# Optimization experiments

Hardware: AMD Instinct MI355X
Metric: run time of the kernel (lower is better)

The kernel has to match this reference:

```python
import jax, jax.numpy as jnp
import numpy as np

N_GENE, N_DIS = 100_000, 50_000   # node counts per node type
D = 128                            # hidden_channels (= input dim, required by skipsum)
E = 800_000                        # edges per edge type
L = 2                              # num_layers
EPS = 1e-12                        # torch F.normalize eps


def setup_inputs() -> dict:
    key = jax.random.key(0)
    ks = jax.random.split(key, 9)
    s = 1.0 / np.sqrt(D)
    return {
        "x_gene": jax.random.normal(ks[0], (N_GENE, D), jnp.float32),
        "x_disease": jax.random.normal(ks[1], (N_DIS, D), jnp.float32),
        # per (layer, edge_type) SAGEConv weights: lin_l (neighbors), lin_r (root), bias
        # edge_type 0: gene->disease, edge_type 1: disease->gene
        "Wl": jax.random.normal(ks[2], (L, 2, D, D), jnp.float32) * s,
        "Wr": jax.random.normal(ks[3], (L, 2, D, D), jnp.float32) * s,
        "b": jax.random.normal(ks[4], (L, 2, D), jnp.float32) * 0.01,
        "src_g2d": jax.random.randint(ks[5], (E,), 0, N_GENE, dtype=jnp.int32),
        "dst_g2d": jax.random.randint(ks[6], (E,), 0, N_DIS, dtype=jnp.int32),
        "src_d2g": jax.random.randint(ks[7], (E,), 0, N_DIS, dtype=jnp.int32),
        "dst_d2g": jax.random.randint(ks[8], (E,), 0, N_GENE, dtype=jnp.int32),
    }


def _sage(x_src, x_dst, src, dst, Wl, Wr, b, n_dst):
    # SAGEConv with aggr='mean': lin_l(mean_{j in N(i)} x_j) + lin_r(x_i) + bias
    msg = jnp.take(x_src, src, axis=0)                                   # [E, D] gather
    summed = jax.ops.segment_sum(msg, dst, num_segments=n_dst)           # [n_dst, D]
    cnt = jax.ops.segment_sum(jnp.ones_like(src, dtype=x_src.dtype), dst,
                              num_segments=n_dst)                        # [n_dst]
    mean = summed / jnp.maximum(cnt, 1.0)[:, None]                       # isolated nodes -> 0
    return mean @ Wl.T + x_dst @ Wr.T + b


def _l2norm(x):
    n = jnp.linalg.norm(x, axis=-1, keepdims=True)
    return x / jnp.maximum(n, EPS)


def reference(x_gene, x_disease, Wl, Wr, b, src_g2d, dst_g2d, src_d2g, dst_d2g):
    xg, xd = x_gene, x_disease
    for i in range(L):
        # to_hetero: one conv per edge type; macro_aggregation='sum' across edge types
        # (each dst type here receives exactly one edge type)
        hd = _sage(xg, xd, src_g2d, dst_g2d, Wl[i, 0], Wr[i, 0], b[i, 0], N_DIS)
        hg = _sage(xd, xg, src_d2g, dst_d2g, Wl[i, 1], Wr[i, 1], b[i, 1], N_GENE)
        if i < L - 1:  # hidden layers get the activation
            hg, hd = jax.nn.relu(hg), jax.nn.relu(hd)
        # L2_norm=True -> normalize every layer
        hg, hd = _l2norm(hg), _l2norm(hd)
        # skipsum
        xg, xd = hg + xg, hd + xd
    return xg, xd
```

## Files before the change

kernel.cpp:

```cpp
#include <hip/hip_runtime.h>
#include <math.h>

#define NG 100000
#define ND 50000
#define NTOT 150000
#define DIM 128
#define NE 800000
#define EPSN 1e-12f

#define RPB 256
#define NBT_D2 196
#define NBT_G2 391

#define NBK 586
#define SCB 128
#define EPB 12500

typedef __bf16 bf16x8 __attribute__((ext_vector_type(8)));
typedef float f32x4 __attribute__((ext_vector_type(4)));
typedef unsigned int uint32;

__device__ __forceinline__ ushort rne_bf16(float f) {
  uint32 u = __builtin_bit_cast(uint32, f);
  u += 0x7fffu + ((u >> 16) & 1u);
  return (ushort)(u >> 16);
}


__global__ void zero_ints(int* __restrict__ p, int n) {
  int i = blockIdx.x * 256 + threadIdx.x;
  if (i < n) p[i] = 0;
}

__global__ void bucket_count(const int* __restrict__ dst_g2d, const int* __restrict__ dst_d2g,
                             int* __restrict__ bcnt) {
  __shared__ int h[NBK];
  for (int j = threadIdx.x; j < NBK; j += 256) h[j] = 0;
  __syncthreads();
  int stride = gridDim.x * 256;
  for (int i = blockIdx.x * 256 + threadIdx.x; i < 2 * NE; i += stride) {
    int d = (i < NE) ? dst_g2d[i] : ND + dst_d2g[i - NE];
    atomicAdd(&h[d >> 8], 1);
  }
  __syncthreads();
  for (int j = threadIdx.x; j < NBK; j += 256)
    if (h[j]) atomicAdd(&bcnt[j], h[j]);
}

__global__ void bucket_scan(const int* __restrict__ bcnt, int* __restrict__ bbase,
                            int* __restrict__ bcur) {
  __shared__ int s[1024];
  int t = threadIdx.x;
  s[t] = (t < NBK) ? bcnt[t] : 0;
  __syncthreads();
  for (int off = 1; off < 1024; off <<= 1) {
    int v = (t >= off) ? s[t - off] : 0;
    __syncthreads();
    s[t] += v;
    __syncthreads();
  }
  if (t < NBK) {
    int e = (t > 0) ? s[t - 1] : 0;
    bbase[t] = e;
    bcur[t] = e;
  }
  if (t == 0) bbase[NBK] = 2 * NE;
}

__global__ void bucket_scatter(const int* __restrict__ src_g2d, const int* __restrict__ dst_g2d,
                               const int* __restrict__ src_d2g, const int* __restrict__ dst_d2g,
                               int* __restrict__ bcur, int2* __restrict__ pairs) {
  __shared__ int h[NBK];
  __shared__ int base[NBK];
  int e0 = blockIdx.x * EPB;
  int e1 = e0 + EPB;
  if (e1 > 2 * NE) e1 = 2 * NE;
  for (int j = threadIdx.x; j < NBK; j += 256) h[j] = 0;
  __syncthreads();
  for (int i = e0 + threadIdx.x; i < e1; i += 256) {
    int d = (i < NE) ? dst_g2d[i] : ND + dst_d2g[i - NE];
    atomicAdd(&h[d >> 8], 1);
  }
  __syncthreads();
  for (int j = threadIdx.x; j < NBK; j += 256) {
    int c = h[j];
    base[j] = c ? atomicAdd(&bcur[j], c) : 0;
    h[j] = 0;
  }
  __syncthreads();
  for (int i = e0 + threadIdx.x; i < e1; i += 256) {
    int d, s;
    if (i < NE) {
      d = dst_g2d[i];
      s = src_g2d[i];
    } else {
      d = ND + dst_d2g[i - NE];
      s = src_d2g[i - NE];
    }
    int bkt = d >> 8;
    int p = base[bkt] + atomicAdd(&h[bkt], 1);
    pairs[p] = make_int2(d, s);
  }
}

__global__ void bucket_to_csr(const int* __restrict__ bbase, const int2* __restrict__ pairs,
                              int* __restrict__ off, int* __restrict__ csr) {
  __shared__ int cnt[256];
  __shared__ int ss[256];
  int b = blockIdx.x, t = threadIdx.x;
  int n0 = b << 8;
  int s0 = bbase[b], s1 = bbase[b + 1];
  cnt[t] = 0;
  __syncthreads();
  for (int i = s0 + t; i < s1; i += 256) atomicAdd(&cnt[pairs[i].x - n0], 1);
  __syncthreads();
  int x = cnt[t];
  ss[t] = x;
  __syncthreads();
  for (int o = 1; o < 256; o <<= 1) {
    int y = (t >= o) ? ss[t - o] : 0;
    __syncthreads();
    ss[t] += y;
    __syncthreads();
  }
  int abs0 = s0 + ss[t] - x;
  int node = n0 + t;
  if (node < NTOT) off[node] = abs0;
  if (node == NTOT - 1) off[NTOT] = 2 * NE;
  __syncthreads();
  cnt[t] = abs0;
  __syncthreads();
  for (int i = s0 + t; i < s1; i += 256) {
    int2 e = pairs[i];
    int p = atomicAdd(&cnt[e.x - n0], 1);
    csr[p] = e.y;
  }
}


__global__ void to_bf16_all(const float* __restrict__ xg, const float* __restrict__ xd,
                            ushort* __restrict__ yg, ushort* __restrict__ yd) {
  int i = blockIdx.x * 256 + threadIdx.x;
  if (i >= NTOT * 16) return;
  const float* x;
  ushort* y;
  int j;
  if (i < NG * 16) {
    x = xg; y = yg; j = i;
  } else {
    x = xd; y = yd; j = i - NG * 16;
  }
  const float4* px = (const float4*)x;
  float4 a = px[2 * j], b = px[2 * j + 1];
  float v[8] = {a.x, a.y, a.z, a.w, b.x, b.y, b.z, b.w};
  uint32 u[4];
#pragma unroll
  for (int k = 0; k < 4; k++)
    u[k] = (uint32)rne_bf16(v[2 * k]) | ((uint32)rne_bf16(v[2 * k + 1]) << 16);
  ((int4*)y)[j] = make_int4((int)u[0], (int)u[1], (int)u[2], (int)u[3]);
}


__global__ void split_w(const float* __restrict__ Wl, const float* __restrict__ Wr,
                        ushort* __restrict__ WlH, ushort* __restrict__ WlL,
                        ushort* __restrict__ WrH, ushort* __restrict__ WrL) {
  int i = blockIdx.x * 256 + threadIdx.x;
  if (i >= 4 * 128 * 128) return;
  {
    float a = Wl[i];
    uint32 u = __builtin_bit_cast(uint32, a);
    float hf = __builtin_bit_cast(float, u & 0xffff0000u);
    WlH[i] = (ushort)(u >> 16);
    WlL[i] = (ushort)(__builtin_bit_cast(uint32, a - hf) >> 16);
  }
  {
    float a = Wr[i];
    uint32 u = __builtin_bit_cast(uint32, a);
    float hf = __builtin_bit_cast(float, u & 0xffff0000u);
    WrH[i] = (ushort)(u >> 16);
    WrL[i] = (ushort)(__builtin_bit_cast(uint32, a - hf) >> 16);
  }
}


__device__ __forceinline__ void acc8(float* a, int4 u) {
  uint32 w;
  w = (uint32)u.x;
  a[0] += __builtin_bit_cast(float, w << 16);
  a[1] += __builtin_bit_cast(float, w & 0xffff0000u);
  w = (uint32)u.y;
  a[2] += __builtin_bit_cast(float, w << 16);
  a[3] += __builtin_bit_cast(float, w & 0xffff0000u);
  w = (uint32)u.z;
  a[4] += __builtin_bit_cast(float, w << 16);
  a[5] += __builtin_bit_cast(float, w & 0xffff0000u);
  w = (uint32)u.w;
  a[6] += __builtin_bit_cast(float, w << 16);
  a[7] += __builtin_bit_cast(float, w & 0xffff0000u);
}

__global__ void agg_comb(const ushort* __restrict__ xg_bf, const ushort* __restrict__ xd_bf,
                         const int* __restrict__ off, const int* __restrict__ csr,
                         ushort* __restrict__ agg_bf) {
  int node = (blockIdx.x * 256 + threadIdx.x) >> 6;
  if (node >= NTOT) return;
  int lane = threadIdx.x & 63;
  const ushort* xsrc = (node < ND) ? xg_bf : xd_bf;
  int e0 = off[node], e1 = off[node + 1];
  int q = lane >> 4, l16 = lane & 15;
  const int4* xs = (const int4*)xsrc;
  float a[8] = {0.f, 0.f, 0.f, 0.f, 0.f, 0.f, 0.f, 0.f};
  int e = e0 + q;
  for (; e + 4 < e1; e += 8) {
    int s0 = csr[e], s1 = csr[e + 4];
    int4 u = xs[(size_t)s0 * 16 + l16];
    int4 v = xs[(size_t)s1 * 16 + l16];
    acc8(a, u);
    acc8(a, v);
  }
  if (e < e1) acc8(a, xs[(size_t)csr[e] * 16 + l16]);
#pragma unroll
  for (int j = 0; j < 8; j++) {
    a[j] += __shfl_xor(a[j], 16);
    a[j] += __shfl_xor(a[j], 32);
  }
  if (q == 0) {
    int deg = e1 - e0;
    float inv = (deg > 0) ? 1.f / (float)deg : 0.f;
    uint32 u[4];
#pragma unroll
    for (int j = 0; j < 4; j++)
      u[j] = (uint32)rne_bf16(a[2 * j] * inv) | ((uint32)rne_bf16(a[2 * j + 1] * inv) << 16);
    *(int4*)&agg_bf[(size_t)node * DIM + l16 * 8] =
        make_int4((int)u[0], (int)u[1], (int)u[2], (int)u[3]);
  }
}


__device__ __forceinline__ void split8(const float* xp, bf16x8& hi, bf16x8& lo) {
  float4 f0 = *(const float4*)xp;
  float4 f1 = *(const float4*)(xp + 4);
  float v[8] = {f0.x, f0.y, f0.z, f0.w, f1.x, f1.y, f1.z, f1.w};
  uint32 hw[4], lw[4];
#pragma unroll
  for (int j = 0; j < 4; j++) {
    uint32 u0 = __builtin_bit_cast(uint32, v[2 * j]);
    uint32 u1 = __builtin_bit_cast(uint32, v[2 * j + 1]);
    float hf0 = __builtin_bit_cast(float, u0 & 0xffff0000u);
    float hf1 = __builtin_bit_cast(float, u1 & 0xffff0000u);
    uint32 l0 = __builtin_bit_cast(uint32, v[2 * j] - hf0) >> 16;
    uint32 l1 = __builtin_bit_cast(uint32, v[2 * j + 1] - hf1) >> 16;
    hw[j] = (u0 >> 16) | ((u1 >> 16) << 16);
    lw[j] = l0 | (l1 << 16);
  }
  hi = __builtin_bit_cast(bf16x8, make_int4((int)hw[0], (int)hw[1], (int)hw[2], (int)hw[3]));
  lo = __builtin_bit_cast(bf16x8, make_int4((int)lw[0], (int)lw[1], (int)lw[2], (int)lw[3]));
}

__launch_bounds__(256, 1)
__global__ void sage_dual(const ushort* __restrict__ agg_bf, const float* __restrict__ xd,
                          const float* __restrict__ xg, const ushort* __restrict__ WlH,
                          const ushort* __restrict__ WlL, const ushort* __restrict__ WrH,
                          const ushort* __restrict__ WrL, const float* __restrict__ bias_all,
                          float* __restrict__ outd, float* __restrict__ outg,
                          ushort* __restrict__ xbf_d, ushort* __restrict__ xbf_g, int layer,
                          int relu, int write_bf) {
  __shared__ __align__(16) char smem[131072];

  int b = blockIdx.x;
  const float* X;
  float* O;
  ushort* OBF;
  int n, set, r0g, cbase;
  if (b < NBT_D2) {
    X = xd; O = outd; OBF = xbf_d; n = ND; set = layer * 2; r0g = b * RPB; cbase = 0;
  } else {
    X = xg; O = outg; OBF = xbf_g; n = NG; set = layer * 2 + 1;
    r0g = (b - NBT_D2) * RPB; cbase = ND;
  }
  const ushort* Wplanes[4] = {WlH + set * 16384, WlL + set * 16384, WrH + set * 16384,
                              WrL + set * 16384};
  const float* bias = bias_all + set * 128;

  int tid = threadIdx.x;
  int wave = tid >> 6, lane = tid & 63;
  int m = lane & 15, q = lane >> 4;

#pragma unroll
  for (int i = 0; i < 32; i++) {
    int c = tid + i * 256;
    int p = c >> 11;
    int Bl = (c & 2047) * 16;
    int4 v = *(const int4*)((const char*)Wplanes[p] + Bl);
    int dst = p * 32768 + (Bl ^ (((Bl >> 8) & 7) << 4));
    *(int4*)(smem + dst) = v;
  }
  __syncthreads();

  f32x4 acc[4][8];
#pragma unroll
  for (int mt = 0; mt < 4; mt++)
#pragma unroll
    for (int nt = 0; nt < 8; nt++) acc[mt][nt] = (f32x4)0.f;

  int rb = r0g + wave * 64;

#pragma unroll
  for (int ks = 0; ks < 4; ks++) {
    int kc = ks * 32 + q * 8;
    int kb = ks * 64 + q * 16;
    bf16x8 a[4];
#pragma unroll
    for (int mt = 0; mt < 4; mt++) {
      int r = rb + mt * 16 + m;
      if (r >= n) r = n - 1;
      a[mt] = __builtin_bit_cast(bf16x8, *(const int4*)&agg_bf[(size_t)(cbase + r) * DIM + kc]);
    }
#pragma unroll
    for (int nt = 0; nt < 8; nt++) {
      int nn = nt * 16 + m;
      int wb = (nn * 256 + kb) ^ ((nn & 7) << 4);
      bf16x8 bh = *(const bf16x8*)(smem + wb);
      bf16x8 bl = *(const bf16x8*)(smem + 32768 + wb);
#pragma unroll
      for (int mt = 0; mt < 4; mt++) {
        acc[mt][nt] = __builtin_amdgcn_mfma_f32_16x16x32_bf16(a[mt], bh, acc[mt][nt], 0, 0, 0);
        acc[mt][nt] = __builtin_amdgcn_mfma_f32_16x16x32_bf16(a[mt], bl, acc[mt][nt], 0, 0, 0);
      }
    }
  }

#pragma unroll
  for (int ks = 0; ks < 4; ks++) {
    int kc = ks * 32 + q * 8;
    int kb = ks * 64 + q * 16;
    bf16x8 ah[4], al[4];
#pragma unroll
    for (int mt = 0; mt < 4; mt++) {
      int r = rb + mt * 16 + m;
      if (r >= n) r = n - 1;
      split8(&X[(size_t)r * DIM + kc], ah[mt], al[mt]);
    }
#pragma unroll
    for (int nt = 0; nt < 8; nt++) {
      int nn = nt * 16 + m;
      int wb = (nn * 256 + kb) ^ ((nn & 7) << 4);
      bf16x8 bh = *(const bf16x8*)(smem + 65536 + wb);
      bf16x8 bl = *(const bf16x8*)(smem + 98304 + wb);
#pragma unroll
      for (int mt = 0; mt < 4; mt++) {
        acc[mt][nt] = __builtin_amdgcn_mfma_f32_16x16x32_bf16(ah[mt], bh, acc[mt][nt], 0, 0, 0);
        acc[mt][nt] = __builtin_amdgcn_mfma_f32_16x16x32_bf16(ah[mt], bl, acc[mt][nt], 0, 0, 0);
        acc[mt][nt] = __builtin_amdgcn_mfma_f32_16x16x32_bf16(al[mt], bh, acc[mt][nt], 0, 0, 0);
      }
    }
  }

  __syncthreads();

  float bb[8];
#pragma unroll
  for (int nt = 0; nt < 8; nt++) bb[nt] = bias[nt * 16 + m];

  const int S = 132;
  float* wbuf = (float*)smem + wave * (16 * S);

  int half = lane >> 5;
  int c4 = (lane & 31) * 4;

#pragma unroll
  for (int mt = 0; mt < 4; mt++) {
#pragma unroll
    for (int reg = 0; reg < 4; reg++) {
      float h[8];
      float ss = 0.f;
#pragma unroll
      for (int nt = 0; nt < 8; nt++) {
        float v = acc[mt][nt][reg] + bb[nt];
        if (relu) v = fmaxf(v, 0.f);
        h[nt] = v;
        ss += v * v;
      }
      ss += __shfl_xor(ss, 1);
      ss += __shfl_xor(ss, 2);
      ss += __shfl_xor(ss, 4);
      ss += __shfl_xor(ss, 8);
      float inv = 1.f / fmaxf(sqrtf(ss), EPSN);
      int rrel = q * 4 + reg;
#pragma unroll
      for (int nt = 0; nt < 8; nt++) wbuf[rrel * S + nt * 16 + m] = h[nt] * inv;
    }
#pragma unroll
    for (int i = 0; i < 8; i++) {
      int rrel = i * 2 + half;
      int R = rb + mt * 16 + rrel;
      if (R < n) {
        f32x4 hv = *(const f32x4*)&wbuf[rrel * S + c4];
        float4 xr = *(const float4*)&X[(size_t)R * DIM + c4];
        float4 o;
        o.x = hv[0] + xr.x;
        o.y = hv[1] + xr.y;
        o.z = hv[2] + xr.z;
        o.w = hv[3] + xr.w;
        *(float4*)&O[(size_t)R * DIM + c4] = o;
        if (write_bf) {
          int2 pk = make_int2((int)((uint32)rne_bf16(o.x) | ((uint32)rne_bf16(o.y) << 16)),
                              (int)((uint32)rne_bf16(o.z) | ((uint32)rne_bf16(o.w) << 16)));
          *(int2*)&OBF[(size_t)R * DIM + c4] = pk;
        }
      }
    }
  }
}


extern "C" void kernel_launch(void* const* d_in, const int* in_sizes, int n_in,
                              void* d_out, int out_size, void* d_ws, size_t ws_size,
                              hipStream_t stream) {
  const float* xg0 = (const float*)d_in[0];
  const float* xd0 = (const float*)d_in[1];
  const float* Wl = (const float*)d_in[2];
  const float* Wr = (const float*)d_in[3];
  const float* bs = (const float*)d_in[4];
  const int* src_g2d = (const int*)d_in[5];
  const int* dst_g2d = (const int*)d_in[6];
  const int* src_d2g = (const int*)d_in[7];
  const int* dst_d2g = (const int*)d_in[8];

  float* out_xg = (float*)d_out;
  float* out_xd = (float*)d_out + (size_t)NG * DIM;

  char* p = (char*)d_ws;
  auto alloc = [&](size_t bytes) -> char* {
    char* q = p;
    p += (bytes + 255) & ~(size_t)255;
    return q;
  };
  int* off = (int*)alloc((NTOT + 1) * 4);
  int* csr = (int*)alloc((size_t)2 * NE * 4);
  int* bcnt = (int*)alloc(NBK * 4);
  int* bbase = (int*)alloc((NBK + 1) * 4);
  int* bcur = (int*)alloc(NBK * 4);
  char* big = alloc((size_t)NTOT * DIM * 2);
  int2* pairs = (int2*)big;
  ushort* agg_bf = (ushort*)big;
  ushort* xg_bf = (ushort*)alloc((size_t)NG * DIM * 2);
  ushort* xd_bf = (ushort*)alloc((size_t)ND * DIM * 2);
  ushort* WlH = (ushort*)alloc((size_t)4 * 128 * 128 * 2);
  ushort* WlL = (ushort*)alloc((size_t)4 * 128 * 128 * 2);
  ushort* WrH = (ushort*)alloc((size_t)4 * 128 * 128 * 2);
  ushort* WrL = (ushort*)alloc((size_t)4 * 128 * 128 * 2);

  const int TB = 256;

  split_w<<<256, TB, 0, stream>>>(Wl, Wr, WlH, WlL, WrH, WrL);
  to_bf16_all<<<(NTOT * 16 + TB - 1) / TB, TB, 0, stream>>>(xg0, xd0, xg_bf, xd_bf);

  zero_ints<<<(NBK + TB - 1) / TB, TB, 0, stream>>>(bcnt, NBK);
  bucket_count<<<256, TB, 0, stream>>>(dst_g2d, dst_d2g, bcnt);
  bucket_scan<<<1, 1024, 0, stream>>>(bcnt, bbase, bcur);
  bucket_scatter<<<SCB, TB, 0, stream>>>(src_g2d, dst_g2d, src_d2g, dst_d2g, bcur, pairs);
  bucket_to_csr<<<NBK, TB, 0, stream>>>(bbase, pairs, off, csr);

  int aggBlocks = NTOT / 4;
  int sageBlocks = NBT_D2 + NBT_G2;

  agg_comb<<<aggBlocks, TB, 0, stream>>>(xg_bf, xd_bf, off, csr, agg_bf);
  sage_dual<<<sageBlocks, TB, 0, stream>>>(agg_bf, xd0, xg0, WlH, WlL, WrH, WrL, bs, out_xd,
                                           out_xg, xd_bf, xg_bf, 0, 1, 1);

  agg_comb<<<aggBlocks, TB, 0, stream>>>(xg_bf, xd_bf, off, csr, agg_bf);
  sage_dual<<<sageBlocks, TB, 0, stream>>>(agg_bf, out_xd, out_xg, WlH, WlL, WrH, WrL, bs,
                                           out_xd, out_xg, xd_bf, xg_bf, 1, 0, 0);
}
```

Before: 539.3 us.

## Use 16 lanes per node in aggregation and halve sage LDS for two blocks/CU

The aggregation kernel now assigns one 16-lane group per destination node instead of a full 64-lane wave, walking edges sequentially with 4-way unrolled gathers and no cross-lane shuffle reduction. The sage_dual kernel stages only the Wl planes into shared memory first, then restages the Wr planes into the same 64 KB buffer, with extra barriers in between. Halving the LDS footprint and raising launch_bounds to 2 blocks per CU is meant to improve occupancy and latency hiding. The cost is an extra weight reload and more barriers per block, plus tighter register limits that could cause spills.

Measured after the change: 483.6 us. 1.12x faster.

```diff
diff --git a/kernel.cpp b/kernel.cpp
--- a/kernel.cpp
+++ b/kernel.cpp
@@ -202,38 +202,40 @@
 __global__ void agg_comb(const ushort* __restrict__ xg_bf, const ushort* __restrict__ xd_bf,
                          const int* __restrict__ off, const int* __restrict__ csr,
                          ushort* __restrict__ agg_bf) {
-  int node = (blockIdx.x * 256 + threadIdx.x) >> 6;
+  int node = (blockIdx.x * 256 + threadIdx.x) >> 4;
   if (node >= NTOT) return;
-  int lane = threadIdx.x & 63;
-  const ushort* xsrc = (node < ND) ? xg_bf : xd_bf;
+  int l16 = threadIdx.x & 15;
+  const int4* xs = (const int4*)((node < ND) ? xg_bf : xd_bf);
   int e0 = off[node], e1 = off[node + 1];
-  int q = lane >> 4, l16 = lane & 15;
-  const int4* xs = (const int4*)xsrc;
   float a[8] = {0.f, 0.f, 0.f, 0.f, 0.f, 0.f, 0.f, 0.f};
-  int e = e0 + q;
-  for (; e + 4 < e1; e += 8) {
-    int s0 = csr[e], s1 = csr[e + 4];
-    int4 u = xs[(size_t)s0 * 16 + l16];
-    int4 v = xs[(size_t)s1 * 16 + l16];
-    acc8(a, u);
-    acc8(a, v);
+  int e = e0;
+  for (; e + 3 < e1; e += 4) {
+    int s0 = csr[e], s1 = csr[e + 1], s2 = csr[e + 2], s3 = csr[e + 3];
+    int4 v0 = xs[(size_t)s0 * 16 + l16];
+    int4 v1 = xs[(size_t)s1 * 16 + l16];
+    int4 v2 = xs[(size_t)s2 * 16 + l16];
+    int4 v3 = xs[(size_t)s3 * 16 + l16];
+    acc8(a, v0);
+    acc8(a, v1);
+    acc8(a, v2);
+    acc8(a, v3);
+  }
+  for (; e + 1 < e1; e += 2) {
+    int s0 = csr[e], s1 = csr[e + 1];
+    int4 v0 = xs[(size_t)s0 * 16 + l16];
+    int4 v1 = xs[(size_t)s1 * 16 + l16];
+    acc8(a, v0);
+    acc8(a, v1);
   }
   if (e < e1) acc8(a, xs[(size_t)csr[e] * 16 + l16]);
-#pragma unroll
-  for (int j = 0; j < 8; j++) {
-    a[j] += __shfl_xor(a[j], 16);
-    a[j] += __shfl_xor(a[j], 32);
-  }
-  if (q == 0) {
-    int deg = e1 - e0;
-    float inv = (deg > 0) ? 1.f / (float)deg : 0.f;
-    uint32 u[4];
-#pragma unroll
-    for (int j = 0; j < 4; j++)
-      u[j] = (uint32)rne_bf16(a[2 * j] * inv) | ((uint32)rne_bf16(a[2 * j + 1] * inv) << 16);
-    *(int4*)&agg_bf[(size_t)node * DIM + l16 * 8] =
-        make_int4((int)u[0], (int)u[1], (int)u[2], (int)u[3]);
-  }
+  int deg = e1 - e0;
+  float inv = (deg > 0) ? 1.f / (float)deg : 0.f;
+  uint32 u[4];
+#pragma unroll
+  for (int j = 0; j < 4; j++)
+    u[j] = (uint32)rne_bf16(a[2 * j] * inv) | ((uint32)rne_bf16(a[2 * j + 1] * inv) << 16);
+  *(int4*)&agg_bf[(size_t)node * DIM + l16 * 8] =
+      make_int4((int)u[0], (int)u[1], (int)u[2], (int)u[3]);
 }
 
 
@@ -257,7 +259,7 @@
   lo = __builtin_bit_cast(bf16x8, make_int4((int)lw[0], (int)lw[1], (int)lw[2], (int)lw[3]));
 }
 
-__launch_bounds__(256, 1)
+__launch_bounds__(256, 2)
 __global__ void sage_dual(const ushort* __restrict__ agg_bf, const float* __restrict__ xd,
                           const float* __restrict__ xg, const ushort* __restrict__ WlH,
                           const ushort* __restrict__ WlL, const ushort* __restrict__ WrH,
@@ -265,7 +267,7 @@
                           float* __restrict__ outd, float* __restrict__ outg,
                           ushort* __restrict__ xbf_d, ushort* __restrict__ xbf_g, int layer,
                           int relu, int write_bf) {
-  __shared__ __align__(16) char smem[131072];
+  __shared__ __align__(16) char smem[65536];
 
   int b = blockIdx.x;
   const float* X;
@@ -286,16 +288,18 @@
   int wave = tid >> 6, lane = tid & 63;
   int m = lane & 15, q = lane >> 4;
 
-#pragma unroll
-  for (int i = 0; i < 32; i++) {
-    int c = tid + i * 256;
-    int p = c >> 11;
-    int Bl = (c & 2047) * 16;
-    int4 v = *(const int4*)((const char*)Wplanes[p] + Bl);
-    int dst = p * 32768 + (Bl ^ (((Bl >> 8) & 7) << 4));
-    *(int4*)(smem + dst) = v;
-  }
-  __syncthreads();
+  auto stageW = [&](const ushort* Ph, const ushort* Pl) {
+#pragma unroll
+    for (int i = 0; i < 16; i++) {
+      int c = tid + i * 256;
+      int p = c >> 11;
+      int Bl = (c & 2047) * 16;
+      const ushort* src = p ? Pl : Ph;
+      int4 v = *(const int4*)((const char*)src + Bl);
+      int dst = p * 32768 + (Bl ^ (((Bl >> 8) & 7) << 4));
+      *(int4*)(smem + dst) = v;
+    }
+  };
 
   f32x4 acc[4][8];
 #pragma unroll
@@ -305,6 +309,8 @@
 
   int rb = r0g + wave * 64;
 
+  stageW(Wplanes[0], Wplanes[1]);
+  __syncthreads();
 #pragma unroll
   for (int ks = 0; ks < 4; ks++) {
     int kc = ks * 32 + q * 8;
@@ -329,7 +335,10 @@
       }
     }
   }
-
+  __syncthreads();
+
+  stageW(Wplanes[2], Wplanes[3]);
+  __syncthreads();
 #pragma unroll
   for (int ks = 0; ks < 4; ks++) {
     int kc = ks * 32 + q * 8;
@@ -345,8 +354,8 @@
     for (int nt = 0; nt < 8; nt++) {
       int nn = nt * 16 + m;
       int wb = (nn * 256 + kb) ^ ((nn & 7) << 4);
-      bf16x8 bh = *(const bf16x8*)(smem + 65536 + wb);
-      bf16x8 bl = *(const bf16x8*)(smem + 98304 + wb);
+      bf16x8 bh = *(const bf16x8*)(smem + wb);
+      bf16x8 bl = *(const bf16x8*)(smem + 32768 + wb);
 #pragma unroll
       for (int mt = 0; mt < 4; mt++) {
         acc[mt][nt] = __builtin_amdgcn_mfma_f32_16x16x32_bf16(ah[mt], bh, acc[mt][nt], 0, 0, 0);
@@ -355,7 +364,6 @@
       }
     }
   }
-
   __syncthreads();
 
   float bb[8];
@@ -462,7 +470,7 @@
   bucket_scatter<<<SCB, TB, 0, stream>>>(src_g2d, dst_g2d, src_d2g, dst_d2g, bcur, pairs);
   bucket_to_csr<<<NBK, TB, 0, stream>>>(bbase, pairs, off, csr);
 
-  int aggBlocks = NTOT / 4;
+  int aggBlocks = (NTOT * 16 + TB - 1) / TB;
   int sageBlocks = NBT_D2 + NBT_G2;
 
   agg_comb<<<aggBlocks, TB, 0, stream>>>(xg_bf, xd_bf, off, csr, agg_bf);
```
